# Kernel optimization log

Hardware: AMD Instinct MI355X
Metric: run time of the kernel (lower is better)

## Reference

```python
import jax, jax.numpy as jnp
import numpy as np

B, T, S, D, H, DK = 2, 2048, 2048, 1024, 16, 64


def setup_inputs() -> dict:
    key = jax.random.key(0)
    ks = jax.random.split(key, 11)
    s = 1.0 / np.sqrt(D)
    return {
        "query": jax.random.normal(ks[0], (B, T, D), jnp.float32),
        "value": jax.random.normal(ks[1], (B, S, D), jnp.float32),
        "key": jax.random.normal(ks[2], (B, S, D), jnp.float32),
        "Wq": jax.random.normal(ks[3], (D, H, DK), jnp.float32) * s,
        "bq": jnp.zeros((H, DK), jnp.float32),
        "Wk": jax.random.normal(ks[4], (D, H, DK), jnp.float32) * s,
        "bk": jnp.zeros((H, DK), jnp.float32),
        "Wv": jax.random.normal(ks[5], (D, H, DK), jnp.float32) * s,
        "bv": jnp.zeros((H, DK), jnp.float32),
        "Wo": jax.random.normal(ks[6], (H, DK, D), jnp.float32) * (1.0 / np.sqrt(H * DK)),
        "bo": jnp.zeros((D,), jnp.float32),
    }


def reference(query, value, key, Wq, bq, Wk, bk, Wv, bv, Wo, bo):
    # Projections: (B, seq, D) x (D, H, DK) -> (B, seq, H, DK)
    q = jnp.einsum("btd,dhk->bthk", query, Wq) + bq
    k = jnp.einsum("bsd,dhk->bshk", key, Wk) + bk
    v = jnp.einsum("bsd,dhk->bshk", value, Wv) + bv
    # Scaled dot-product attention (keras scales query by 1/sqrt(key_dim))
    q = q * (1.0 / np.sqrt(DK)).astype(np.float32)
    scores = jnp.einsum("bshk,bthk->bhts", k, q)  # (B, H, T, S)
    probs = jax.nn.softmax(scores, axis=-1)
    attn = jnp.einsum("bhts,bshk->bthk", probs, v)  # (B, T, H, DK)
    # Output projection back to model dim
    out = jnp.einsum("bthk,hkd->btd", attn, Wo) + bo
    return out
```

## Files before the change

### kernel.cpp

```cpp
#include <hip/hip_runtime.h>
#include <math.h>

#define BB  2
#define TT  2048
#define SSQ 2048
#define DD  1024
#define HH  16
#define DKK 64
#define MM  (BB*TT)
#define NN  (HH*DKK)

typedef __attribute__((ext_vector_type(8))) short short8;
typedef __attribute__((ext_vector_type(4))) float f32x4;
typedef __attribute__((ext_vector_type(2))) unsigned int uint2v;
typedef __attribute__((ext_vector_type(4))) unsigned int u32x4;

__device__ __forceinline__ short f2bf(float x) {
    unsigned u = __builtin_bit_cast(unsigned, x);
    unsigned r = (u + 0x7FFFu + ((u >> 16) & 1u)) >> 16;
    return (short)r;
}

__device__ __forceinline__ unsigned pk2(float lo, float hi) {
    return (__builtin_bit_cast(unsigned, hi) & 0xFFFF0000u) |
           (__builtin_bit_cast(unsigned, lo) >> 16);
}

__device__ __forceinline__ void glds16(const void* g, void* l) {
    __builtin_amdgcn_global_load_lds(
        (const __attribute__((address_space(1))) void*)g,
        (__attribute__((address_space(3))) void*)l, 16, 0, 0);
}

__global__ __launch_bounds__(256)
void to_bf16_acts(const float* __restrict__ a0, const float* __restrict__ a1,
                  const float* __restrict__ a2,
                  short* __restrict__ o0, short* __restrict__ o1,
                  short* __restrict__ o2)
{
    int z = blockIdx.y;
    const float* in = (z == 0) ? a0 : (z == 1) ? a1 : a2;
    short* out = (z == 0) ? o0 : (z == 1) ? o1 : o2;
    size_t i0 = ((size_t)blockIdx.x * 256 + threadIdx.x) * 8;
    f32x4 f0 = *(const f32x4*)(in + i0);
    f32x4 f1 = *(const f32x4*)(in + i0 + 4);
    short8 v;
#pragma unroll
    for (int j = 0; j < 4; j++) v[j] = f2bf(f0[j]);
#pragma unroll
    for (int j = 0; j < 4; j++) v[4 + j] = f2bf(f1[j]);
    *(short8*)(out + i0) = v;
}

__global__ __launch_bounds__(256)
void wtrans(const float* __restrict__ w0, const float* __restrict__ w1,
            const float* __restrict__ w2, const float* __restrict__ w3,
            short* __restrict__ t0, short* __restrict__ t1,
            short* __restrict__ t2, short* __restrict__ t3)
{
    __shared__ float Ls[64][65];
    int z = blockIdx.z;
    const float* in = (z == 0) ? w0 : (z == 1) ? w1 : (z == 2) ? w2 : w3;
    short* out = (z == 0) ? t0 : (z == 1) ? t1 : (z == 2) ? t2 : t3;
    const int r0 = blockIdx.y * 64, c0 = blockIdx.x * 64;
    const int t = threadIdx.x;
    const int r = t >> 2, c4 = t & 3;

    const float* src = in + (size_t)(r0 + r) * DD + c0 + c4 * 16;
#pragma unroll
    for (int i = 0; i < 4; i++) {
        f32x4 f = *(const f32x4*)(src + i * 4);
#pragma unroll
        for (int j = 0; j < 4; j++) Ls[r][c4 * 16 + i * 4 + j] = f[j];
    }
    __syncthreads();

    short8 va, vb;
#pragma unroll
    for (int j = 0; j < 8; j++) va[j] = f2bf(Ls[c4 * 16 + j][r]);
#pragma unroll
    for (int j = 0; j < 8; j++) vb[j] = f2bf(Ls[c4 * 16 + 8 + j][r]);
    short* dst = out + (size_t)(c0 + r) * DD + r0 + c4 * 16;
    *(short8*)dst = va;
    *(short8*)(dst + 8) = vb;
}

__global__ __launch_bounds__(256)
void vtrans(const short* __restrict__ in, short* __restrict__ out)
{
    __shared__ short Ls[64][72];
    const int bh = blockIdx.y;
    const int t0 = blockIdx.x * 64;
    const int tid = threadIdx.x;
    const int r = tid >> 2, c4 = tid & 3;

    const short* src = in + ((size_t)bh * TT + t0 + r) * DKK + c4 * 16;
    *(short8*)&Ls[r][c4 * 16]     = *(const short8*)(src);
    *(short8*)&Ls[r][c4 * 16 + 8] = *(const short8*)(src + 8);
    __syncthreads();

    short8 a, b;
#pragma unroll
    for (int j = 0; j < 8; j++) a[j] = Ls[c4 * 16 + j][r];
#pragma unroll
    for (int j = 0; j < 8; j++) b[j] = Ls[c4 * 16 + 8 + j][r];
    short* dst = out + ((size_t)bh * DKK + r) * SSQ + t0 + c4 * 16;
    *(short8*)dst = a;
    *(short8*)(dst + 8) = b;
}

__device__ __forceinline__ void gemm_core(const short* __restrict__ A,
                                          const short* __restrict__ Bt,
                                          int m0, int n0,
                                          short* As, short* Bs,
                                          f32x4 (&acc)[4][4])
{
    const int tid = threadIdx.x;
    const int w = tid >> 6, l = tid & 63;
    const int l15 = l & 15, quad = l >> 4;
    const int wm = w >> 1, wn = w & 1;

#pragma unroll
    for (int i = 0; i < 4; i++)
#pragma unroll
        for (int j = 0; j < 4; j++) acc[i][j] = (f32x4){0.f, 0.f, 0.f, 0.f};

    const int r = tid >> 2, cseg = tid & 3;
    const short* gA = A + (size_t)(m0 + r) * DD + cseg * 8;
    const short* gB = Bt + (size_t)(n0 + r) * DD + cseg * 8;
    short* ldsA = As + w * 512;
    short* ldsB = Bs + w * 512;

    for (int k0 = 0; k0 < DD; k0 += 32) {
        glds16(gA + k0,                 ldsA);
        glds16(gA + (size_t)64 * DD + k0, ldsA + 2048);
        glds16(gB + k0,                 ldsB);
        glds16(gB + (size_t)64 * DD + k0, ldsB + 2048);
        __syncthreads();

        short8 bF[4];
#pragma unroll
        for (int ni = 0; ni < 4; ni++)
            bF[ni] = *(const short8*)&Bs[(wn * 64 + ni * 16 + l15) * 32 + quad * 8];
#pragma unroll
        for (int mi = 0; mi < 4; mi++) {
            short8 aF = *(const short8*)&As[(wm * 64 + mi * 16 + l15) * 32 + quad * 8];
#pragma unroll
            for (int ni = 0; ni < 4; ni++)
                acc[mi][ni] = __builtin_amdgcn_mfma_f32_16x16x32_bf16(aF, bF[ni], acc[mi][ni], 0, 0, 0);
        }
        __syncthreads();
    }
}

__global__ __launch_bounds__(256, 3)
void gemm_qkv(const short* __restrict__ Aq, const short* __restrict__ Ak,
              const short* __restrict__ Av,
              const short* __restrict__ Wqt, const short* __restrict__ Wkt,
              const short* __restrict__ Wvt,
              const float* __restrict__ bq, const float* __restrict__ bk,
              const float* __restrict__ bv,
              short* __restrict__ Qb, short* __restrict__ Kb,
              short* __restrict__ Vtmp)
{
    __shared__ short As[128 * 32];
    __shared__ short Bs[128 * 32];
    const int z = blockIdx.z;
    const short* A  = (z == 0) ? Aq : (z == 1) ? Ak : Av;
    const short* Bt = (z == 0) ? Wqt : (z == 1) ? Wkt : Wvt;
    const float* bias = (z == 0) ? bq : (z == 1) ? bk : bv;
    short* dst = (z == 0) ? Qb : (z == 1) ? Kb : Vtmp;
    const int m0 = blockIdx.y * 128, n0 = blockIdx.x * 128;

    f32x4 acc[4][4];
    gemm_core(A, Bt, m0, n0, As, Bs, acc);

    const int tid = threadIdx.x;
    const int w = tid >> 6, l = tid & 63;
    const int l15 = l & 15, quad = l >> 4;
    const int wm = w >> 1, wn = w & 1;
    const float scale = (z == 0) ? 0.1803368801f : 1.0f;

#pragma unroll
    for (int mi = 0; mi < 4; mi++) {
#pragma unroll
        for (int reg = 0; reg < 4; reg++) {
            int m = m0 + wm * 64 + mi * 16 + quad * 4 + reg;
            int b = m >> 11, t = m & 2047;
#pragma unroll
            for (int ni = 0; ni < 4; ni++) {
                int n = n0 + wn * 64 + ni * 16 + l15;
                float vv = (acc[mi][ni][reg] + bias[n]) * scale;
                int h = n >> 6, dk = n & 63;
                dst[((size_t)(b * HH + h) * TT + t) * DKK + dk] = f2bf(vv);
            }
        }
    }
}

__global__ __launch_bounds__(256, 3)
void gemm_out(const short* __restrict__ Ab, const short* __restrict__ Wot,
              const float* __restrict__ bo, float* __restrict__ out)
{
    __shared__ short As[128 * 32];
    __shared__ short Bs[128 * 32];
    const int m0 = blockIdx.y * 128, n0 = blockIdx.x * 128;

    f32x4 acc[4][4];
    gemm_core(Ab, Wot, m0, n0, As, Bs, acc);

    const int tid = threadIdx.x;
    const int w = tid >> 6, l = tid & 63;
    const int l15 = l & 15, quad = l >> 4;
    const int wm = w >> 1, wn = w & 1;

#pragma unroll
    for (int mi = 0; mi < 4; mi++) {
#pragma unroll
        for (int reg = 0; reg < 4; reg++) {
            int m = m0 + wm * 64 + mi * 16 + quad * 4 + reg;
#pragma unroll
            for (int ni = 0; ni < 4; ni++) {
                int n = n0 + wn * 64 + ni * 16 + l15;
                out[(size_t)m * DD + n] = acc[mi][ni][reg] + bo[n];
            }
        }
    }
}

__global__ __launch_bounds__(512, 4)
void attn_mfma(const short* __restrict__ Qb, const short* __restrict__ Kb,
               const short* __restrict__ Vbt, short* __restrict__ Ab)
{
    __shared__ short KV[2 * 2 * 2 * 64 * 72];

    const int tid = threadIdx.x;
    const int w = tid >> 6, l = tid & 63;
    const int wq = w & 3, half = w >> 2;
    const int l15 = l & 15, quad = l >> 4;
    const int bh = blockIdx.y;
    const int t0 = blockIdx.x * 128;
    const size_t hb = (size_t)bh * SSQ * DKK;
    const int th = tid & 255;
    const int r = th >> 2, c4 = th & 3;

    short8 qf[2][2];
#pragma unroll
    for (int mf = 0; mf < 2; mf++)
#pragma unroll
        for (int kk = 0; kk < 2; kk++)
            qf[mf][kk] = *(const short8*)(Qb + hb +
                (size_t)(t0 + 32 * wq + 16 * mf + l15) * DKK + kk * 32 + quad * 8);

    const short* gkb = Kb + hb + (size_t)(half * 1024 + r) * DKK + c4 * 16;
    const short* gvb = Vbt + hb + (size_t)r * SSQ + half * 1024 + c4 * 16;
    short8 kr0 = *(const short8*)(gkb + 0);
    short8 kr1 = *(const short8*)(gkb + 8);
    short8 vr0 = *(const short8*)(gvb + 0);
    short8 vr1 = *(const short8*)(gvb + 8);

    f32x4 o[2][4];
#pragma unroll
    for (int mf = 0; mf < 2; mf++)
#pragma unroll
        for (int j = 0; j < 4; j++) o[mf][j] = (f32x4){0.f, 0.f, 0.f, 0.f};
    float lsum[2] = {0.f, 0.f};

    short* skb = KV + half * 18432 + r * 72 + c4 * 16;
    const short* khalf0 = KV + half * 18432;

    for (int s0 = 0; s0 < 1024; s0 += 64) {
        const int dbo = (s0 & 64) ? 9216 : 0;
        *(short8*)(skb + dbo)          = kr0;
        *(short8*)(skb + dbo + 8)      = kr1;
        *(short8*)(skb + dbo + 4608)   = vr0;
        *(short8*)(skb + dbo + 4616)   = vr1;
        if (s0 + 64 < 1024) {
            const short* gk = gkb + (size_t)(s0 + 64) * DKK;
            const short* gv = gvb + (s0 + 64);
            kr0 = *(const short8*)(gk + 0);
            kr1 = *(const short8*)(gk + 8);
            vr0 = *(const short8*)(gv + 0);
            vr1 = *(const short8*)(gv + 8);
        }
        __syncthreads();
        const short* kb_ = khalf0 + dbo;
        const short* vb_ = kb_ + 4608;

        f32x4 sc[4][2];
#pragma unroll
        for (int np = 0; np < 4; np++)
#pragma unroll
            for (int mf = 0; mf < 2; mf++) sc[np][mf] = (f32x4){0.f, 0.f, 0.f, 0.f};
        __builtin_amdgcn_s_setprio(1);
#pragma unroll
        for (int kk = 0; kk < 2; kk++) {
#pragma unroll
            for (int np = 0; np < 4; np++) {
                short8 aK = *(const short8*)&kb_[(16 * np + l15) * 72 + kk * 32 + quad * 8];
                sc[np][0] = __builtin_amdgcn_mfma_f32_16x16x32_bf16(aK, qf[0][kk], sc[np][0], 0, 0, 0);
                sc[np][1] = __builtin_amdgcn_mfma_f32_16x16x32_bf16(aK, qf[1][kk], sc[np][1], 0, 0, 0);
            }
        }
        __builtin_amdgcn_s_setprio(0);

        short8 pa[2][2];
#pragma unroll
        for (int mf = 0; mf < 2; mf++) {
            float pe[4][4];
            float ls = lsum[mf];
#pragma unroll
            for (int np = 0; np < 4; np++) {
#pragma unroll
                for (int reg = 0; reg < 4; reg++) {
                    float p = __builtin_amdgcn_exp2f(sc[np][mf][reg]);
                    pe[np][reg] = p;
                    ls += p;
                }
            }
            lsum[mf] = ls;
#pragma unroll
            for (int kk = 0; kk < 2; kk++) {
                u32x4 wd;
#pragma unroll
                for (int b = 0; b < 2; b++) {
                    unsigned Xw = pk2(pe[2 * kk][2 * b],     pe[2 * kk][2 * b + 1]);
                    unsigned Yw = pk2(pe[2 * kk + 1][2 * b], pe[2 * kk + 1][2 * b + 1]);
                    uint2v s1 = __builtin_amdgcn_permlane32_swap(Xw, Yw, false, false);
                    uint2v s2 = __builtin_amdgcn_permlane16_swap(s1[0], s1[1], false, false);
                    wd[b]     = s2[0];
                    wd[2 + b] = s2[1];
                }
                pa[mf][kk] = __builtin_bit_cast(short8, wd);
            }
        }

        __builtin_amdgcn_s_setprio(1);
#pragma unroll
        for (int kk = 0; kk < 2; kk++) {
#pragma unroll
            for (int np = 0; np < 4; np++) {
                short8 bV = *(const short8*)&vb_[(16 * np + l15) * 72 + kk * 32 + quad * 8];
                o[0][np] = __builtin_amdgcn_mfma_f32_16x16x32_bf16(pa[0][kk], bV, o[0][np], 0, 0, 0);
                o[1][np] = __builtin_amdgcn_mfma_f32_16x16x32_bf16(pa[1][kk], bV, o[1][np], 0, 0, 0);
            }
        }
        __builtin_amdgcn_s_setprio(0);
    }

    __syncthreads();
    float* F = (float*)KV;
    const int slot = (wq * 64 + l) * 36;
    if (half == 1) {
#pragma unroll
        for (int mf = 0; mf < 2; mf++)
#pragma unroll
            for (int np = 0; np < 4; np++)
                *(f32x4*)&F[slot + (mf * 4 + np) * 4] = o[mf][np];
        F[slot + 32] = lsum[0];
        F[slot + 33] = lsum[1];
    }
    __syncthreads();
    if (half == 0) {
#pragma unroll
        for (int mf = 0; mf < 2; mf++) {
#pragma unroll
            for (int np = 0; np < 4; np++) {
                f32x4 po = *(const f32x4*)&F[slot + (mf * 4 + np) * 4];
                o[mf][np] += po;
            }
            lsum[mf] += F[slot + 32 + mf];
        }

        const int b = bh >> 4, h = bh & 15;
#pragma unroll
        for (int mf = 0; mf < 2; mf++) {
            float ls = lsum[mf];
            ls += __shfl_xor(ls, 16);
            ls += __shfl_xor(ls, 32);
            float inv = 1.f / ls;
#pragma unroll
            for (int reg = 0; reg < 4; reg++) {
                float invr = __shfl(inv, quad * 4 + reg);
                int t = t0 + 32 * wq + 16 * mf + quad * 4 + reg;
#pragma unroll
                for (int np = 0; np < 4; np++) {
                    Ab[((size_t)(b * TT + t) * HH + h) * DKK + 16 * np + l15] =
                        f2bf(o[mf][np][reg] * invr);
                }
            }
        }
    }
}

extern "C" void kernel_launch(void* const* d_in, const int* in_sizes, int n_in,
                              void* d_out, int out_size, void* d_ws, size_t ws_size,
                              hipStream_t stream)
{
    const float* query = (const float*)d_in[0];
    const float* value = (const float*)d_in[1];
    const float* key   = (const float*)d_in[2];
    const float* Wq    = (const float*)d_in[3];
    const float* bq    = (const float*)d_in[4];
    const float* Wk    = (const float*)d_in[5];
    const float* bk    = (const float*)d_in[6];
    const float* Wv    = (const float*)d_in[7];
    const float* bv    = (const float*)d_in[8];
    const float* Wo    = (const float*)d_in[9];
    const float* bo    = (const float*)d_in[10];
    float* out = (float*)d_out;

    const size_t actE = (size_t)MM * DD;
    const size_t wE   = (size_t)DD * NN;
    short* p = (short*)d_ws;
    short* Aq   = p; p += actE;
    short* Ak   = p; p += actE;
    short* Av   = p; p += actE;
    short* Wqt  = p; p += wE;
    short* Wkt  = p; p += wE;
    short* Wvt  = p; p += wE;
    short* Wot  = p; p += wE;
    short* Qb   = p; p += actE;
    short* Kb   = p; p += actE;
    short* Vtmp = p; p += actE;
    short* Vbt  = p; p += actE;
    short* Ab   = p; p += actE;

    dim3 blk(256);

    to_bf16_acts<<<dim3((unsigned)(actE / 2048), 3), blk, 0, stream>>>(
        query, key, value, Aq, Ak, Av);

    wtrans<<<dim3(16, 16, 4), blk, 0, stream>>>(Wq, Wk, Wv, Wo, Wqt, Wkt, Wvt, Wot);

    gemm_qkv<<<dim3(NN / 128, MM / 128, 3), blk, 0, stream>>>(
        Aq, Ak, Av, Wqt, Wkt, Wvt, bq, bk, bv, Qb, Kb, Vtmp);

    vtrans<<<dim3(TT / 64, BB * HH), blk, 0, stream>>>(Vtmp, Vbt);

    attn_mfma<<<dim3(TT / 128, BB * HH), dim3(512), 0, stream>>>(Qb, Kb, Vbt, Ab);

    gemm_out<<<dim3(DD / 128, MM / 128), blk, 0, stream>>>(Ab, Wot, bo, out);
}
```

Measured before the change: 235.3 us.

## Load K/V MFMA operands directly from global memory and swizzle block order

Removes the LDS double-buffered staging of K and V tiles and the per-iteration __syncthreads, so each wave reads its MFMA operand fragments straight from global memory (relying on L1/L2 for reuse across the four waves sharing a half). The block index is also remapped with a swizzle so consecutive blocks spread across heads/batches, aiming at better L2 locality across XCDs. LDS shrinks to just the cross-half reduction buffer, which can raise occupancy, but every wave now issues redundant global loads and loses the prefetch overlap that the register staging provided.

```diff
diff --git a/kernel.cpp b/kernel.cpp
--- a/kernel.cpp
+++ b/kernel.cpp
@@ -232,17 +232,18 @@
 void attn_mfma(const short* __restrict__ Qb, const short* __restrict__ Kb,
                const short* __restrict__ Vbt, short* __restrict__ Ab)
 {
-    __shared__ short KV[2 * 2 * 2 * 64 * 72];
+    __shared__ float F[256 * 36];
 
     const int tid = threadIdx.x;
     const int w = tid >> 6, l = tid & 63;
     const int wq = w & 3, half = w >> 2;
     const int l15 = l & 15, quad = l >> 4;
-    const int bh = blockIdx.y;
-    const int t0 = blockIdx.x * 128;
+
+    const int fid = blockIdx.y * 16 + blockIdx.x;
+    const int swz = (fid & 7) * 64 + (fid >> 3);
+    const int t0 = (swz & 15) * 128;
+    const int bh = swz >> 4;
     const size_t hb = (size_t)bh * SSQ * DKK;
-    const int th = tid & 255;
-    const int r = th >> 2, c4 = th & 3;
 
     short8 qf[2][2];
 #pragma unroll
@@ -252,12 +253,8 @@
             qf[mf][kk] = *(const short8*)(Qb + hb +
                 (size_t)(t0 + 32 * wq + 16 * mf + l15) * DKK + kk * 32 + quad * 8);
 
-    const short* gkb = Kb + hb + (size_t)(half * 1024 + r) * DKK + c4 * 16;
-    const short* gvb = Vbt + hb + (size_t)r * SSQ + half * 1024 + c4 * 16;
-    short8 kr0 = *(const short8*)(gkb + 0);
-    short8 kr1 = *(const short8*)(gkb + 8);
-    short8 vr0 = *(const short8*)(gvb + 0);
-    short8 vr1 = *(const short8*)(gvb + 8);
+    const short* kRow = Kb + hb + (size_t)(half * 1024 + l15) * DKK + quad * 8;
+    const short* vRow = Vbt + hb + (size_t)l15 * SSQ + half * 1024 + quad * 8;
 
     f32x4 o[2][4];
 #pragma unroll
@@ -266,27 +263,7 @@
         for (int j = 0; j < 4; j++) o[mf][j] = (f32x4){0.f, 0.f, 0.f, 0.f};
     float lsum[2] = {0.f, 0.f};
 
-    short* skb = KV + half * 18432 + r * 72 + c4 * 16;
-    const short* khalf0 = KV + half * 18432;
-
     for (int s0 = 0; s0 < 1024; s0 += 64) {
-        const int dbo = (s0 & 64) ? 9216 : 0;
-        *(short8*)(skb + dbo)          = kr0;
-        *(short8*)(skb + dbo + 8)      = kr1;
-        *(short8*)(skb + dbo + 4608)   = vr0;
-        *(short8*)(skb + dbo + 4616)   = vr1;
-        if (s0 + 64 < 1024) {
-            const short* gk = gkb + (size_t)(s0 + 64) * DKK;
-            const short* gv = gvb + (s0 + 64);
-            kr0 = *(const short8*)(gk + 0);
-            kr1 = *(const short8*)(gk + 8);
-            vr0 = *(const short8*)(gv + 0);
-            vr1 = *(const short8*)(gv + 8);
-        }
-        __syncthreads();
-        const short* kb_ = khalf0 + dbo;
-        const short* vb_ = kb_ + 4608;
-
         f32x4 sc[4][2];
 #pragma unroll
         for (int np = 0; np < 4; np++)
@@ -297,7 +274,7 @@
         for (int kk = 0; kk < 2; kk++) {
 #pragma unroll
             for (int np = 0; np < 4; np++) {
-                short8 aK = *(const short8*)&kb_[(16 * np + l15) * 72 + kk * 32 + quad * 8];
+                short8 aK = *(const short8*)(kRow + (size_t)(s0 + 16 * np) * DKK + kk * 32);
                 sc[np][0] = __builtin_amdgcn_mfma_f32_16x16x32_bf16(aK, qf[0][kk], sc[np][0], 0, 0, 0);
                 sc[np][1] = __builtin_amdgcn_mfma_f32_16x16x32_bf16(aK, qf[1][kk], sc[np][1], 0, 0, 0);
             }
@@ -340,7 +317,7 @@
         for (int kk = 0; kk < 2; kk++) {
 #pragma unroll
             for (int np = 0; np < 4; np++) {
-                short8 bV = *(const short8*)&vb_[(16 * np + l15) * 72 + kk * 32 + quad * 8];
+                short8 bV = *(const short8*)(vRow + (size_t)(16 * np) * SSQ + s0 + kk * 32);
                 o[0][np] = __builtin_amdgcn_mfma_f32_16x16x32_bf16(pa[0][kk], bV, o[0][np], 0, 0, 0);
                 o[1][np] = __builtin_amdgcn_mfma_f32_16x16x32_bf16(pa[1][kk], bV, o[1][np], 0, 0, 0);
             }
@@ -349,7 +326,6 @@
     }
 
     __syncthreads();
-    float* F = (float*)KV;
     const int slot = (wq * 64 + l) * 36;
     if (half == 1) {
 #pragma unroll
```

Measured after the change: 302.5 us. 28.5% more time.

## Drop split-S attention halves, use 256-thread blocks with swizzled block order

Applied to the files above, without the earlier changes.

The attention kernel no longer splits the key sequence between two 4-wave halves of a 512-thread block. Each 256-thread block now walks the full sequence, which removes the LDS reduction and the extra barriers at the end. Block indices are swizzled so neighbouring blocks map to different heads, and the exp2 calls are interleaved with the bf16 packing to shorten register lifetimes. The trade-off is half as many waves per query tile and twice the serial loop length, leaving less parallelism to hide latency.

```diff
diff --git a/kernel.cpp b/kernel.cpp
--- a/kernel.cpp
+++ b/kernel.cpp
@@ -228,21 +228,22 @@
     }
 }
 
-__global__ __launch_bounds__(512, 4)
+__global__ __launch_bounds__(256, 3)
 void attn_mfma(const short* __restrict__ Qb, const short* __restrict__ Kb,
                const short* __restrict__ Vbt, short* __restrict__ Ab)
 {
-    __shared__ short KV[2 * 2 * 2 * 64 * 72];
+    __shared__ short KV[2 * 2 * 64 * 72];
 
     const int tid = threadIdx.x;
     const int w = tid >> 6, l = tid & 63;
-    const int wq = w & 3, half = w >> 2;
     const int l15 = l & 15, quad = l >> 4;
-    const int bh = blockIdx.y;
-    const int t0 = blockIdx.x * 128;
+
+    const int fid = blockIdx.y * 16 + blockIdx.x;
+    const int swz = (fid & 7) * 64 + (fid >> 3);
+    const int t0 = (swz & 15) * 128;
+    const int bh = swz >> 4;
     const size_t hb = (size_t)bh * SSQ * DKK;
-    const int th = tid & 255;
-    const int r = th >> 2, c4 = th & 3;
+    const int r = tid >> 2, c4 = tid & 3;
 
     short8 qf[2][2];
 #pragma unroll
@@ -250,10 +251,10 @@
 #pragma unroll
         for (int kk = 0; kk < 2; kk++)
             qf[mf][kk] = *(const short8*)(Qb + hb +
-                (size_t)(t0 + 32 * wq + 16 * mf + l15) * DKK + kk * 32 + quad * 8);
-
-    const short* gkb = Kb + hb + (size_t)(half * 1024 + r) * DKK + c4 * 16;
-    const short* gvb = Vbt + hb + (size_t)r * SSQ + half * 1024 + c4 * 16;
+                (size_t)(t0 + 32 * w + 16 * mf + l15) * DKK + kk * 32 + quad * 8);
+
+    const short* gkb = Kb + hb + (size_t)r * DKK + c4 * 16;
+    const short* gvb = Vbt + hb + (size_t)r * SSQ + c4 * 16;
     short8 kr0 = *(const short8*)(gkb + 0);
     short8 kr1 = *(const short8*)(gkb + 8);
     short8 vr0 = *(const short8*)(gvb + 0);
@@ -266,16 +267,15 @@
         for (int j = 0; j < 4; j++) o[mf][j] = (f32x4){0.f, 0.f, 0.f, 0.f};
     float lsum[2] = {0.f, 0.f};
 
-    short* skb = KV + half * 18432 + r * 72 + c4 * 16;
-    const short* khalf0 = KV + half * 18432;
-
-    for (int s0 = 0; s0 < 1024; s0 += 64) {
+    short* skb = KV + r * 72 + c4 * 16;
+
+    for (int s0 = 0; s0 < SSQ; s0 += 64) {
         const int dbo = (s0 & 64) ? 9216 : 0;
         *(short8*)(skb + dbo)          = kr0;
         *(short8*)(skb + dbo + 8)      = kr1;
         *(short8*)(skb + dbo + 4608)   = vr0;
         *(short8*)(skb + dbo + 4616)   = vr1;
-        if (s0 + 64 < 1024) {
+        if (s0 + 64 < SSQ) {
             const short* gk = gkb + (size_t)(s0 + 64) * DKK;
             const short* gv = gvb + (s0 + 64);
             kr0 = *(const short8*)(gk + 0);
@@ -284,7 +284,7 @@
             vr1 = *(const short8*)(gv + 8);
         }
         __syncthreads();
-        const short* kb_ = khalf0 + dbo;
+        const short* kb_ = KV + dbo;
         const short* vb_ = kb_ + 4608;
 
         f32x4 sc[4][2];
@@ -307,25 +307,19 @@
         short8 pa[2][2];
 #pragma unroll
         for (int mf = 0; mf < 2; mf++) {
-            float pe[4][4];
             float ls = lsum[mf];
-#pragma unroll
-            for (int np = 0; np < 4; np++) {
-#pragma unroll
-                for (int reg = 0; reg < 4; reg++) {
-                    float p = __builtin_amdgcn_exp2f(sc[np][mf][reg]);
-                    pe[np][reg] = p;
-                    ls += p;
-                }
-            }
-            lsum[mf] = ls;
 #pragma unroll
             for (int kk = 0; kk < 2; kk++) {
                 u32x4 wd;
 #pragma unroll
                 for (int b = 0; b < 2; b++) {
-                    unsigned Xw = pk2(pe[2 * kk][2 * b],     pe[2 * kk][2 * b + 1]);
-                    unsigned Yw = pk2(pe[2 * kk + 1][2 * b], pe[2 * kk + 1][2 * b + 1]);
+                    float p00 = __builtin_amdgcn_exp2f(sc[2 * kk][mf][2 * b]);
+                    float p01 = __builtin_amdgcn_exp2f(sc[2 * kk][mf][2 * b + 1]);
+                    float p10 = __builtin_amdgcn_exp2f(sc[2 * kk + 1][mf][2 * b]);
+                    float p11 = __builtin_amdgcn_exp2f(sc[2 * kk + 1][mf][2 * b + 1]);
+                    ls += (p00 + p01) + (p10 + p11);
+                    unsigned Xw = pk2(p00, p01);
+                    unsigned Yw = pk2(p10, p11);
                     uint2v s1 = __builtin_amdgcn_permlane32_swap(Xw, Yw, false, false);
                     uint2v s2 = __builtin_amdgcn_permlane16_swap(s1[0], s1[1], false, false);
                     wd[b]     = s2[0];
@@ -333,6 +327,7 @@
                 }
                 pa[mf][kk] = __builtin_bit_cast(short8, wd);
             }
+            lsum[mf] = ls;
         }
 
         __builtin_amdgcn_s_setprio(1);
@@ -348,46 +343,21 @@
         __builtin_amdgcn_s_setprio(0);
     }
 
-    __syncthreads();
-    float* F = (float*)KV;
-    const int slot = (wq * 64 + l) * 36;
-    if (half == 1) {
-#pragma unroll
-        for (int mf = 0; mf < 2; mf++)
-#pragma unroll
-            for (int np = 0; np < 4; np++)
-                *(f32x4*)&F[slot + (mf * 4 + np) * 4] = o[mf][np];
-        F[slot + 32] = lsum[0];
-        F[slot + 33] = lsum[1];
-    }
-    __syncthreads();
-    if (half == 0) {
-#pragma unroll
-        for (int mf = 0; mf < 2; mf++) {
+    const int b = bh >> 4, h = bh & 15;
+#pragma unroll
+    for (int mf = 0; mf < 2; mf++) {
+        float ls = lsum[mf];
+        ls += __shfl_xor(ls, 16);
+        ls += __shfl_xor(ls, 32);
+        float inv = 1.f / ls;
+#pragma unroll
+        for (int reg = 0; reg < 4; reg++) {
+            float invr = __shfl(inv, quad * 4 + reg);
+            int t = t0 + 32 * w + 16 * mf + quad * 4 + reg;
 #pragma unroll
             for (int np = 0; np < 4; np++) {
-                f32x4 po = *(const f32x4*)&F[slot + (mf * 4 + np) * 4];
-                o[mf][np] += po;
-            }
-            lsum[mf] += F[slot + 32 + mf];
-        }
-
-        const int b = bh >> 4, h = bh & 15;
-#pragma unroll
-        for (int mf = 0; mf < 2; mf++) {
-            float ls = lsum[mf];
-            ls += __shfl_xor(ls, 16);
-            ls += __shfl_xor(ls, 32);
-            float inv = 1.f / ls;
-#pragma unroll
-            for (int reg = 0; reg < 4; reg++) {
-                float invr = __shfl(inv, quad * 4 + reg);
-                int t = t0 + 32 * wq + 16 * mf + quad * 4 + reg;
-#pragma unroll
-                for (int np = 0; np < 4; np++) {
-                    Ab[((size_t)(b * TT + t) * HH + h) * DKK + 16 * np + l15] =
-                        f2bf(o[mf][np][reg] * invr);
-                }
+                Ab[((size_t)(b * TT + t) * HH + h) * DKK + 16 * np + l15] =
+                    f2bf(o[mf][np][reg] * invr);
             }
         }
     }
@@ -438,7 +408,7 @@
 
     vtrans<<<dim3(TT / 64, BB * HH), blk, 0, stream>>>(Vtmp, Vbt);
 
-    attn_mfma<<<dim3(TT / 128, BB * HH), dim3(512), 0, stream>>>(Qb, Kb, Vbt, Ab);
+    attn_mfma<<<dim3(TT / 128, BB * HH), blk, 0, stream>>>(Qb, Kb, Vbt, Ab);
 
     gemm_out<<<dim3(DD / 128, MM / 128), blk, 0, stream>>>(Ab, Wot, bo, out);
 }
```

After: 233.8 us. No clear change (-0.7%).
